# Kernel tuning notes

Measured on AMD Instinct MI355X. Metric: run time of the kernel, lower is better.

Reference implementation:

```python
import jax, jax.numpy as jnp
import numpy as np

N_CLUSTERS = 256  # must match fill_max of `clusters`
ALPHA = 7.18
MIN_MEMBERS = 4.0  # clusters with fewer members are dropped (as in original)


def setup_inputs() -> dict:
    key = jax.random.key(0)
    k1, k2 = jax.random.split(key)
    outputs = jax.random.normal(k1, (8192, 2048), dtype=jnp.float32)
    clusters = jax.random.randint(k2, (8192,), 0, N_CLUSTERS, dtype=jnp.int32)
    return {"outputs": outputs, "clusters": clusters}


def _magnet_loss(outputs, clusters):
    # outputs: [N, D] float32, clusters: [N] int32 in [0, N_CLUSTERS)
    n = outputs.shape[0]
    ones = jnp.ones((n,), jnp.float32)
    counts = jax.ops.segment_sum(ones, clusters, num_segments=N_CLUSTERS)          # [C]
    sums = jax.ops.segment_sum(outputs, clusters, num_segments=N_CLUSTERS)         # [C, D]
    means = sums / jnp.maximum(counts, 1.0)[:, None]                               # [C, D]
    valid = counts >= MIN_MEMBERS                                                   # [C] clusters kept
    inst_valid = valid[clusters]                                                    # [N]

    # residual norms to own-cluster mean (UNSQUARED L2, as in original)
    resid = outputs - means[clusters]                                               # [N, D]
    resid_norm = jnp.sqrt(jnp.sum(resid * resid, axis=1))                           # [N]

    num_instances = jnp.sum(jnp.where(valid, counts, 0.0))
    # original quirk: stdev = (sum of norms)^2 / num_instances
    stdev = jnp.square(jnp.sum(jnp.where(inst_valid, resid_norm, 0.0))) / num_instances

    # pairwise instance-to-mean L2 distances via GEMM: [N, C]
    sq = (jnp.sum(outputs * outputs, axis=1)[:, None]
          - 2.0 * (outputs @ means.T)
          + jnp.sum(means * means, axis=1)[None, :])
    dist = jnp.sqrt(jnp.maximum(sq, 0.0))                                           # [N, C]

    expd = jnp.exp(-0.5 * dist / stdev)                                             # [N, C]
    # denominator: sum over valid clusters other than own cluster
    other = jnp.arange(N_CLUSTERS, dtype=clusters.dtype)[None, :] != clusters[:, None]
    mask = valid[None, :] & other                                                   # [N, C]
    denom = jnp.sum(jnp.where(mask, expd, 0.0), axis=1)                             # [N]

    log_num = -0.5 * resid_norm / stdev - ALPHA                                     # [N]
    loss_i = jnp.log(denom) - log_num                                               # -log(exp(log_num)/denom)
    loss = jnp.sum(jnp.where(inst_valid, loss_i, 0.0)) / num_instances
    return loss.reshape(1)


def reference(outputs, clusters):
    return _magnet_loss(outputs.astype(jnp.float32), clusters)
```

## Files before the change

### kernel.cpp

```cpp
#include <hip/hip_runtime.h>
#include <hip/hip_bf16.h>
#include <math.h>

#define NROWS 8192
#define DIM   2048
#define NC    256
#define ALPHA_C 7.18f

typedef float  f32x4  __attribute__((ext_vector_type(4)));
typedef __bf16 bf16x8 __attribute__((ext_vector_type(8)));

#define OFF_A      (size_t)0
#define OFF_DOT    ((size_t)32 << 20)
#define OFF_B      ((size_t)40 << 20)
#define OFF_PERM   ((size_t)41 << 20)
#define OFF_MISC   (OFF_PERM + 32768)
#define OFF_GCTR   (OFF_MISC)
#define OFF_MN2    (OFF_MISC + 1024)
#define OFF_SCAL   (OFF_MISC + 2048)
#define OFF_HIST   (OFF_MISC + 3072)
#define OFF_CNT    (OFF_MISC + 4096)
#define OFF_BASE   (OFF_MISC + 5120)
#define OFF_ON2    (OFF_MISC + 6144)

__device__ __forceinline__ float wave_red_sum(float v) {
#pragma unroll
  for (int off = 32; off > 0; off >>= 1) v += __shfl_xor(v, off, 64);
  return v;
}

__global__ __launch_bounds__(256) void k_hist(const int* __restrict__ clu,
                                              int* __restrict__ hist) {
  __shared__ int h[NC];
  int tid = threadIdx.x;
  h[tid] = 0;
  __syncthreads();
  atomicAdd(&h[clu[blockIdx.x * 256 + tid]], 1);
  __syncthreads();
  if (h[tid]) atomicAdd(&hist[tid], h[tid]);
}

__global__ __launch_bounds__(256) void k_scan(const int* __restrict__ hist,
                                              float* __restrict__ counts,
                                              int* __restrict__ base,
                                              float* scal) {
  __shared__ int pre[NC];
  __shared__ float part[4];
  int tid = threadIdx.x;
  int c = hist[tid];
  counts[tid] = (float)c;
  pre[tid] = c;
  __syncthreads();
  for (int off = 1; off < NC; off <<= 1) {
    int v = (tid >= off) ? pre[tid - off] : 0;
    __syncthreads();
    pre[tid] += v;
    __syncthreads();
  }
  base[tid] = pre[tid] - c;
  float v = (c >= 4) ? (float)c : 0.0f;
  v = wave_red_sum(v);
  if ((tid & 63) == 0) part[tid >> 6] = v;
  __syncthreads();
  if (tid == 0) scal[1] = part[0] + part[1] + part[2] + part[3];
}

__global__ __launch_bounds__(256) void k_perm(const int* __restrict__ clu,
                                              const int* __restrict__ base,
                                              int* __restrict__ gctr,
                                              int* __restrict__ perm) {
  int i = blockIdx.x * 256 + threadIdx.x;
  int c = clu[i];
  int r = atomicAdd(&gctr[c], 1);
  perm[base[c] + r] = i;
}

__global__ __launch_bounds__(256) void k_msum(const float* __restrict__ out,
                                              const int* __restrict__ perm,
                                              const int* __restrict__ base,
                                              const float* __restrict__ counts,
                                              __bf16* __restrict__ B,
                                              float* __restrict__ mn2) {
  __shared__ int pr[64];
  __shared__ float part[4];
  int bid = blockIdx.x;
  int c = bid >> 3, sl = bid & 7;
  int tid = threadIdx.x;
  int col = sl * 256 + tid;
  int cnt = (int)counts[c];
  int b0 = base[c];
  float acc = 0.f;
  for (int r0 = 0; r0 < cnt; r0 += 64) {
    int lim = min(64, cnt - r0);
    if (tid < lim) pr[tid] = perm[b0 + r0 + tid];
    __syncthreads();
    for (int r = 0; r < lim; ++r) acc += out[(size_t)pr[r] * DIM + col];
    __syncthreads();
  }
  float mean = acc / fmaxf((float)cnt, 1.f);
  int nt = c >> 4, kk = col >> 5, lane = ((col >> 3) & 3) * 16 + (c & 15), j = col & 7;
  B[(((size_t)nt * 64 + kk) * 64 + lane) * 8 + j] = (__bf16)mean;
  float s = mean * mean;
  s = wave_red_sum(s);
  if ((tid & 63) == 0) part[tid >> 6] = s;
  __syncthreads();
  if (tid == 0) atomicAdd(&mn2[c], part[0] + part[1] + part[2] + part[3]);
}

__global__ __launch_bounds__(256) void k_conv(const float* __restrict__ out,
                                              bf16x8* __restrict__ A,
                                              float* __restrict__ onorm2) {
  __shared__ float lsum[256];
  int mt = blockIdx.x, tid = threadIdx.x;
  int r = tid & 15;
  const float* rowp = out + ((size_t)mt * 16 + r) * DIM;
  bf16x8* At = A + (size_t)mt * 4096;
  float acc = 0.f;
#pragma unroll 4
  for (int s = 0; s < 16; ++s) {
    int q = s * 256 + tid;
    int kk = q >> 6, lane = q & 63;
    int d = kk * 32 + (lane >> 4) * 8;
    const f32x4* src = (const f32x4*)(rowp + d);
    f32x4 v0 = src[0], v1 = src[1];
    bf16x8 b;
#pragma unroll
    for (int j = 0; j < 4; ++j) { float f = v0[j]; acc += f * f; b[j] = (__bf16)f; }
#pragma unroll
    for (int j = 0; j < 4; ++j) { float f = v1[j]; acc += f * f; b[4 + j] = (__bf16)f; }
    At[q] = b;
  }
  lsum[tid] = acc;
  __syncthreads();
  if (tid < 16) {
    float s = 0.f;
#pragma unroll
    for (int k = 0; k < 16; ++k) s += lsum[tid + 16 * k];
    onorm2[mt * 16 + tid] = s;
  }
}

__global__ __launch_bounds__(256) void k_gemm(const bf16x8* __restrict__ A,
                                              const bf16x8* __restrict__ B,
                                              float* __restrict__ dot) {
  int bid = blockIdx.x;
  int wg = (bid & 7) * 32 + (bid >> 3);
  int bm = wg >> 2, bn = wg & 3;
  int w = threadIdx.x >> 6, l = threadIdx.x & 63;
  int mt0 = bm * 8 + w * 2;
  int nt0 = bn * 4;
  const bf16x8* Ap = A + (size_t)mt0 * 64 * 64 + l;
  const bf16x8* Bp = B + (size_t)nt0 * 64 * 64 + l;
  f32x4 acc[2][4] = {};
  for (int kk = 0; kk < 64; ++kk) {
    bf16x8 a0 = Ap[kk * 64];
    bf16x8 a1 = Ap[4096 + kk * 64];
    bf16x8 b0 = Bp[kk * 64];
    bf16x8 b1 = Bp[4096 + kk * 64];
    bf16x8 b2 = Bp[8192 + kk * 64];
    bf16x8 b3 = Bp[12288 + kk * 64];
    acc[0][0] = __builtin_amdgcn_mfma_f32_16x16x32_bf16(a0, b0, acc[0][0], 0, 0, 0);
    acc[0][1] = __builtin_amdgcn_mfma_f32_16x16x32_bf16(a0, b1, acc[0][1], 0, 0, 0);
    acc[0][2] = __builtin_amdgcn_mfma_f32_16x16x32_bf16(a0, b2, acc[0][2], 0, 0, 0);
    acc[0][3] = __builtin_amdgcn_mfma_f32_16x16x32_bf16(a0, b3, acc[0][3], 0, 0, 0);
    acc[1][0] = __builtin_amdgcn_mfma_f32_16x16x32_bf16(a1, b0, acc[1][0], 0, 0, 0);
    acc[1][1] = __builtin_amdgcn_mfma_f32_16x16x32_bf16(a1, b1, acc[1][1], 0, 0, 0);
    acc[1][2] = __builtin_amdgcn_mfma_f32_16x16x32_bf16(a1, b2, acc[1][2], 0, 0, 0);
    acc[1][3] = __builtin_amdgcn_mfma_f32_16x16x32_bf16(a1, b3, acc[1][3], 0, 0, 0);
  }
  int r0 = bm * 128 + w * 32 + (l >> 4) * 4;
  int cb = bn * 64 + (l & 15);
#pragma unroll
  for (int m = 0; m < 2; ++m)
#pragma unroll
    for (int reg = 0; reg < 4; ++reg) {
      float* dst = dot + (size_t)(r0 + m * 16 + reg) * NC + cb;
#pragma unroll
      for (int n = 0; n < 4; ++n) dst[n * 16] = acc[m][n][reg];
    }
}

__global__ __launch_bounds__(256) void k_resid2(const float* __restrict__ dot,
                                                const int* __restrict__ clu,
                                                const float* __restrict__ onorm2,
                                                const float* __restrict__ mnorm2,
                                                const float* __restrict__ counts,
                                                float* scal) {
  __shared__ float part[4];
  int tid = threadIdx.x;
  int i = blockIdx.x * 256 + tid;
  int ci = clu[i];
  float dv = dot[(size_t)i * NC + ci];
  float rn = sqrtf(fmaxf(onorm2[i] - 2.f * dv + mnorm2[ci], 0.f));
  float v = (counts[ci] >= 4.0f) ? rn : 0.f;
  v = wave_red_sum(v);
  if ((tid & 63) == 0) part[tid >> 6] = v;
  __syncthreads();
  if (tid == 0) atomicAdd(&scal[0], part[0] + part[1] + part[2] + part[3]);
}

__global__ void k_stdev(float* scal) {
  scal[2] = scal[0] * scal[0] / scal[1];
}

__global__ __launch_bounds__(256) void k_denom(const float* __restrict__ dot,
                                               const int* __restrict__ clu,
                                               const float* __restrict__ on2v,
                                               const float* __restrict__ mn2,
                                               const float* __restrict__ counts,
                                               float* scal) {
  __shared__ float part[4];
  int w = threadIdx.x >> 6, l = threadIdx.x & 63;
  float cfac = -0.5f / scal[2];
  f32x4 mn = ((const f32x4*)mn2)[l];
  f32x4 cn = ((const f32x4*)counts)[l];
  float lsum = 0.f;
  int i0 = blockIdx.x * 32 + w * 8;
  for (int t = 0; t < 8; ++t) {
    int i = i0 + t;
    int ci = clu[i];
    float on2 = on2v[i];
    f32x4 dv = ((const f32x4*)(dot + (size_t)i * NC))[l];
    float dsum = 0.f;
#pragma unroll
    for (int j = 0; j < 4; ++j) {
      int cc = l * 4 + j;
      float dist = sqrtf(fmaxf(on2 - 2.f * dv[j] + mn[j], 0.f));
      float e = __expf(cfac * dist);
      dsum += ((cn[j] >= 4.0f) && (cc != ci)) ? e : 0.f;
    }
    dsum = wave_red_sum(dsum);
    if (l == 0 && counts[ci] >= 4.0f) {
      float dvi = dot[(size_t)i * NC + ci];
      float rn = sqrtf(fmaxf(on2 - 2.f * dvi + mn2[ci], 0.f));
      lsum += __logf(dsum) - (cfac * rn - ALPHA_C);
    }
  }
  lsum = wave_red_sum(lsum);
  if (l == 0) part[w] = lsum;
  __syncthreads();
  if (threadIdx.x == 0) atomicAdd(&scal[3], part[0] + part[1] + part[2] + part[3]);
}

__global__ void k_final(const float* scal, float* out) {
  out[0] = scal[3] / scal[1];
}

extern "C" void kernel_launch(void* const* d_in, const int* in_sizes, int n_in,
                              void* d_out, int out_size, void* d_ws, size_t ws_size,
                              hipStream_t stream) {
  const float* outputs = (const float*)d_in[0];
  const int* clusters = (const int*)d_in[1];
  float* out = (float*)d_out;
  char* ws = (char*)d_ws;

  bf16x8* A      = (bf16x8*)(ws + OFF_A);
  float*  dotb   = (float*)(ws + OFF_DOT);
  __bf16* B      = (__bf16*)(ws + OFF_B);
  int*    perm   = (int*)(ws + OFF_PERM);
  int*    gctr   = (int*)(ws + OFF_GCTR);
  float*  mn2    = (float*)(ws + OFF_MN2);
  float*  scal   = (float*)(ws + OFF_SCAL);
  int*    hist   = (int*)(ws + OFF_HIST);
  float*  counts = (float*)(ws + OFF_CNT);
  int*    base   = (int*)(ws + OFF_BASE);
  float*  on2    = (float*)(ws + OFF_ON2);

  hipMemsetAsync(ws + OFF_GCTR, 0, 4096, stream);
  k_hist<<<NROWS / 256, 256, 0, stream>>>(clusters, hist);
  k_scan<<<1, 256, 0, stream>>>(hist, counts, base, scal);
  k_perm<<<NROWS / 256, 256, 0, stream>>>(clusters, base, gctr, perm);
  k_conv<<<NROWS / 16, 256, 0, stream>>>(outputs, A, on2);
  k_msum<<<NC * 8, 256, 0, stream>>>(outputs, perm, base, counts, B, mn2);
  k_gemm<<<256, 256, 0, stream>>>(A, (const bf16x8*)B, dotb);
  k_resid2<<<NROWS / 256, 256, 0, stream>>>(dotb, clusters, on2, mn2, counts, scal);
  k_stdev<<<1, 1, 0, stream>>>(scal);
  k_denom<<<NROWS / 32, 256, 0, stream>>>(dotb, clusters, on2, mn2, counts, scal);
  k_final<<<1, 1, 0, stream>>>(scal, out);
}
```

Before: 179.4 us.

## Fuse GEMM, residual, denominator and final loss into one cooperative kernel

Replaces the GEMM, residual-norm, stdev, denominator and final kernels with a single cooperative kernel. It keeps the dot products in MFMA accumulator registers and uses grid syncs between the stdev reduction, the per-row denominator atomics and the final sum. This removes the 8192x256 float dot buffer write and reread, along with several launches. The histogram and scan are also merged into one single-block kernel. In exchange it adds three grid-wide barriers, per-row float atomics on dsum (which makes the sum order nondeterministic), and relies on all 256 blocks being co-resident.

New measurement: 262.3 us. +46.2%, slower.

```diff
diff --git a/kernel.cpp b/kernel.cpp
--- a/kernel.cpp
+++ b/kernel.cpp
@@ -1,6 +1,9 @@
 #include <hip/hip_runtime.h>
 #include <hip/hip_bf16.h>
+#include <hip/hip_cooperative_groups.h>
 #include <math.h>
+
+namespace cg = cooperative_groups;
 
 #define NROWS 8192
 #define DIM   2048
@@ -11,17 +14,18 @@
 typedef __bf16 bf16x8 __attribute__((ext_vector_type(8)));
 
 #define OFF_A      (size_t)0
-#define OFF_DOT    ((size_t)32 << 20)
-#define OFF_B      ((size_t)40 << 20)
-#define OFF_PERM   ((size_t)41 << 20)
-#define OFF_MISC   (OFF_PERM + 32768)
-#define OFF_GCTR   (OFF_MISC)
-#define OFF_MN2    (OFF_MISC + 1024)
-#define OFF_SCAL   (OFF_MISC + 2048)
-#define OFF_HIST   (OFF_MISC + 3072)
-#define OFF_CNT    (OFF_MISC + 4096)
-#define OFF_BASE   (OFF_MISC + 5120)
-#define OFF_ON2    (OFF_MISC + 6144)
+#define OFF_B      ((size_t)32 << 20)
+#define OFF_PERM   ((size_t)33 << 20)
+#define OFF_Z      (OFF_PERM + 32768)
+#define OFF_GCTR   (OFF_Z)
+#define OFF_MN2    (OFF_Z + 1024)
+#define OFF_SCAL   (OFF_Z + 2048)
+#define OFF_DSUM   (OFF_Z + 3072)
+#define ZSIZE      (3072 + 32768)
+#define OFF_CNT    (OFF_Z + ZSIZE)
+#define OFF_BASE   (OFF_CNT + 1024)
+#define OFF_ON2    (OFF_BASE + 1024)
+#define OFF_RN     (OFF_ON2 + 32768)
 
 __device__ __forceinline__ float wave_red_sum(float v) {
 #pragma unroll
@@ -29,25 +33,25 @@
   return v;
 }
 
-__global__ __launch_bounds__(256) void k_hist(const int* __restrict__ clu,
-                                              int* __restrict__ hist) {
-  __shared__ int h[NC];
-  int tid = threadIdx.x;
-  h[tid] = 0;
-  __syncthreads();
-  atomicAdd(&h[clu[blockIdx.x * 256 + tid]], 1);
-  __syncthreads();
-  if (h[tid]) atomicAdd(&hist[tid], h[tid]);
-}
-
-__global__ __launch_bounds__(256) void k_scan(const int* __restrict__ hist,
+__global__ __launch_bounds__(256) void k_prep(const int* __restrict__ clu,
                                               float* __restrict__ counts,
                                               int* __restrict__ base,
                                               float* scal) {
+  __shared__ int h[NC];
   __shared__ int pre[NC];
   __shared__ float part[4];
   int tid = threadIdx.x;
-  int c = hist[tid];
+  h[tid] = 0;
+  __syncthreads();
+  const int4* cl4 = (const int4*)clu;
+#pragma unroll
+  for (int s = 0; s < 8; ++s) {
+    int4 v = cl4[s * 256 + tid];
+    atomicAdd(&h[v.x], 1); atomicAdd(&h[v.y], 1);
+    atomicAdd(&h[v.z], 1); atomicAdd(&h[v.w], 1);
+  }
+  __syncthreads();
+  int c = h[tid];
   counts[tid] = (float)c;
   pre[tid] = c;
   __syncthreads();
@@ -73,6 +77,39 @@
   int c = clu[i];
   int r = atomicAdd(&gctr[c], 1);
   perm[base[c] + r] = i;
+}
+
+__global__ __launch_bounds__(256) void k_conv(const float* __restrict__ out,
+                                              bf16x8* __restrict__ A,
+                                              float* __restrict__ onorm2) {
+  __shared__ float lsum[256];
+  int mt = blockIdx.x, tid = threadIdx.x;
+  int r = tid & 15;
+  const float* rowp = out + ((size_t)mt * 16 + r) * DIM;
+  bf16x8* At = A + (size_t)mt * 4096;
+  float acc = 0.f;
+#pragma unroll 4
+  for (int s = 0; s < 16; ++s) {
+    int q = s * 256 + tid;
+    int kk = q >> 6, lane = q & 63;
+    int d = kk * 32 + (lane >> 4) * 8;
+    const f32x4* src = (const f32x4*)(rowp + d);
+    f32x4 v0 = src[0], v1 = src[1];
+    bf16x8 b;
+#pragma unroll
+    for (int j = 0; j < 4; ++j) { float f = v0[j]; acc += f * f; b[j] = (__bf16)f; }
+#pragma unroll
+    for (int j = 0; j < 4; ++j) { float f = v1[j]; acc += f * f; b[4 + j] = (__bf16)f; }
+    At[q] = b;
+  }
+  lsum[tid] = acc;
+  __syncthreads();
+  if (tid < 16) {
+    float s = 0.f;
+#pragma unroll
+    for (int k = 0; k < 16; ++k) s += lsum[tid + 16 * k];
+    onorm2[mt * 16 + tid] = s;
+  }
 }
 
 __global__ __launch_bounds__(256) void k_msum(const float* __restrict__ out,
@@ -107,42 +144,18 @@
   if (tid == 0) atomicAdd(&mn2[c], part[0] + part[1] + part[2] + part[3]);
 }
 
-__global__ __launch_bounds__(256) void k_conv(const float* __restrict__ out,
-                                              bf16x8* __restrict__ A,
-                                              float* __restrict__ onorm2) {
-  __shared__ float lsum[256];
-  int mt = blockIdx.x, tid = threadIdx.x;
-  int r = tid & 15;
-  const float* rowp = out + ((size_t)mt * 16 + r) * DIM;
-  bf16x8* At = A + (size_t)mt * 4096;
-  float acc = 0.f;
-#pragma unroll 4
-  for (int s = 0; s < 16; ++s) {
-    int q = s * 256 + tid;
-    int kk = q >> 6, lane = q & 63;
-    int d = kk * 32 + (lane >> 4) * 8;
-    const f32x4* src = (const f32x4*)(rowp + d);
-    f32x4 v0 = src[0], v1 = src[1];
-    bf16x8 b;
-#pragma unroll
-    for (int j = 0; j < 4; ++j) { float f = v0[j]; acc += f * f; b[j] = (__bf16)f; }
-#pragma unroll
-    for (int j = 0; j < 4; ++j) { float f = v1[j]; acc += f * f; b[4 + j] = (__bf16)f; }
-    At[q] = b;
-  }
-  lsum[tid] = acc;
-  __syncthreads();
-  if (tid < 16) {
-    float s = 0.f;
-#pragma unroll
-    for (int k = 0; k < 16; ++k) s += lsum[tid + 16 * k];
-    onorm2[mt * 16 + tid] = s;
-  }
-}
-
-__global__ __launch_bounds__(256) void k_gemm(const bf16x8* __restrict__ A,
-                                              const bf16x8* __restrict__ B,
-                                              float* __restrict__ dot) {
+__global__ __launch_bounds__(256) void k_fused(const bf16x8* __restrict__ A,
+                                               const bf16x8* __restrict__ B,
+                                               const int* __restrict__ clu,
+                                               const float* __restrict__ counts,
+                                               const float* __restrict__ on2v,
+                                               const float* __restrict__ mn2,
+                                               float* __restrict__ rn,
+                                               float* __restrict__ dsum,
+                                               float* scal,
+                                               float* outp) {
+  __shared__ float part[4];
+  cg::grid_group grid = cg::this_grid();
   int bid = blockIdx.x;
   int wg = (bid & 7) * 32 + (bid >> 3);
   int bm = wg >> 2, bn = wg & 3;
@@ -170,80 +183,78 @@
   }
   int r0 = bm * 128 + w * 32 + (l >> 4) * 4;
   int cb = bn * 64 + (l & 15);
+
+  int ciArr[8]; float on2Arr[8];
+  float rsum = 0.f;
 #pragma unroll
   for (int m = 0; m < 2; ++m)
 #pragma unroll
     for (int reg = 0; reg < 4; ++reg) {
-      float* dst = dot + (size_t)(r0 + m * 16 + reg) * NC + cb;
-#pragma unroll
-      for (int n = 0; n < 4; ++n) dst[n * 16] = acc[m][n][reg];
+      int idx = m * 4 + reg;
+      int i = r0 + m * 16 + reg;
+      int ci = clu[i];
+      float o2 = on2v[i];
+      ciArr[idx] = ci; on2Arr[idx] = o2;
+#pragma unroll
+      for (int n = 0; n < 4; ++n) {
+        int c = cb + n * 16;
+        if (c == ci) {
+          float v = acc[m][n][reg];
+          float rnv = sqrtf(fmaxf(o2 - 2.f * v + mn2[ci], 0.f));
+          rn[i] = rnv;
+          if (counts[ci] >= 4.f) rsum += rnv;
+        }
+      }
     }
-}
-
-__global__ __launch_bounds__(256) void k_resid2(const float* __restrict__ dot,
-                                                const int* __restrict__ clu,
-                                                const float* __restrict__ onorm2,
-                                                const float* __restrict__ mnorm2,
-                                                const float* __restrict__ counts,
-                                                float* scal) {
-  __shared__ float part[4];
+  rsum = wave_red_sum(rsum);
+  if (l == 0) part[w] = rsum;
+  __syncthreads();
+  if (threadIdx.x == 0) atomicAdd(&scal[0], part[0] + part[1] + part[2] + part[3]);
+  grid.sync();
+
+  float s0 = scal[0], s1 = scal[1];
+  float cfac = -0.5f * s1 / (s0 * s0);
+  float mnc[4], cnc[4];
+#pragma unroll
+  for (int n = 0; n < 4; ++n) { int c = cb + n * 16; mnc[n] = mn2[c]; cnc[n] = counts[c]; }
+#pragma unroll
+  for (int m = 0; m < 2; ++m)
+#pragma unroll
+    for (int reg = 0; reg < 4; ++reg) {
+      int idx = m * 4 + reg;
+      int i = r0 + m * 16 + reg;
+      int ci = ciArr[idx];
+      float o2 = on2Arr[idx];
+      float p = 0.f;
+#pragma unroll
+      for (int n = 0; n < 4; ++n) {
+        int c = cb + n * 16;
+        float v = acc[m][n][reg];
+        float dist = sqrtf(fmaxf(o2 - 2.f * v + mnc[n], 0.f));
+        float e = __expf(cfac * dist);
+        p += ((cnc[n] >= 4.f) && (c != ci)) ? e : 0.f;
+      }
+#pragma unroll
+      for (int off = 1; off < 16; off <<= 1) p += __shfl_xor(p, off, 64);
+      if ((l & 15) == 0) atomicAdd(&dsum[i], p);
+    }
+  grid.sync();
+
+  float lv = 0.f;
   int tid = threadIdx.x;
-  int i = blockIdx.x * 256 + tid;
-  int ci = clu[i];
-  float dv = dot[(size_t)i * NC + ci];
-  float rn = sqrtf(fmaxf(onorm2[i] - 2.f * dv + mnorm2[ci], 0.f));
-  float v = (counts[ci] >= 4.0f) ? rn : 0.f;
-  v = wave_red_sum(v);
-  if ((tid & 63) == 0) part[tid >> 6] = v;
-  __syncthreads();
-  if (tid == 0) atomicAdd(&scal[0], part[0] + part[1] + part[2] + part[3]);
-}
-
-__global__ void k_stdev(float* scal) {
-  scal[2] = scal[0] * scal[0] / scal[1];
-}
-
-__global__ __launch_bounds__(256) void k_denom(const float* __restrict__ dot,
-                                               const int* __restrict__ clu,
-                                               const float* __restrict__ on2v,
-                                               const float* __restrict__ mn2,
-                                               const float* __restrict__ counts,
-                                               float* scal) {
-  __shared__ float part[4];
-  int w = threadIdx.x >> 6, l = threadIdx.x & 63;
-  float cfac = -0.5f / scal[2];
-  f32x4 mn = ((const f32x4*)mn2)[l];
-  f32x4 cn = ((const f32x4*)counts)[l];
-  float lsum = 0.f;
-  int i0 = blockIdx.x * 32 + w * 8;
-  for (int t = 0; t < 8; ++t) {
-    int i = i0 + t;
+  if (tid < 32) {
+    int i = blockIdx.x * 32 + tid;
     int ci = clu[i];
-    float on2 = on2v[i];
-    f32x4 dv = ((const f32x4*)(dot + (size_t)i * NC))[l];
-    float dsum = 0.f;
-#pragma unroll
-    for (int j = 0; j < 4; ++j) {
-      int cc = l * 4 + j;
-      float dist = sqrtf(fmaxf(on2 - 2.f * dv[j] + mn[j], 0.f));
-      float e = __expf(cfac * dist);
-      dsum += ((cn[j] >= 4.0f) && (cc != ci)) ? e : 0.f;
-    }
-    dsum = wave_red_sum(dsum);
-    if (l == 0 && counts[ci] >= 4.0f) {
-      float dvi = dot[(size_t)i * NC + ci];
-      float rn = sqrtf(fmaxf(on2 - 2.f * dvi + mn2[ci], 0.f));
-      lsum += __logf(dsum) - (cfac * rn - ALPHA_C);
-    }
-  }
-  lsum = wave_red_sum(lsum);
-  if (l == 0) part[w] = lsum;
-  __syncthreads();
-  if (threadIdx.x == 0) atomicAdd(&scal[3], part[0] + part[1] + part[2] + part[3]);
-}
-
-__global__ void k_final(const float* scal, float* out) {
-  out[0] = scal[3] / scal[1];
+    if (counts[ci] >= 4.f)
+      lv = __logf(dsum[i]) - (cfac * rn[i] - ALPHA_C);
+  }
+  lv = wave_red_sum(lv);
+  if (l == 0) part[w] = lv;
+  __syncthreads();
+  if (tid == 0) atomicAdd(&scal[3], part[0] + part[1] + part[2] + part[3]);
+  grid.sync();
+
+  if (blockIdx.x == 0 && tid == 0) outp[0] = scal[3] / scal[1];
 }
 
 extern "C" void kernel_launch(void* const* d_in, const int* in_sizes, int n_in,
@@ -251,30 +262,29 @@
                               hipStream_t stream) {
   const float* outputs = (const float*)d_in[0];
   const int* clusters = (const int*)d_in[1];
-  float* out = (float*)d_out;
+  float* outp = (float*)d_out;
   char* ws = (char*)d_ws;
 
   bf16x8* A      = (bf16x8*)(ws + OFF_A);
-  float*  dotb   = (float*)(ws + OFF_DOT);
-  __bf16* B      = (__bf16*)(ws + OFF_B);
+  bf16x8* B      = (bf16x8*)(ws + OFF_B);
   int*    perm   = (int*)(ws + OFF_PERM);
   int*    gctr   = (int*)(ws + OFF_GCTR);
   float*  mn2    = (float*)(ws + OFF_MN2);
   float*  scal   = (float*)(ws + OFF_SCAL);
-  int*    hist   = (int*)(ws + OFF_HIST);
+  float*  dsum   = (float*)(ws + OFF_DSUM);
   float*  counts = (float*)(ws + OFF_CNT);
   int*    base   = (int*)(ws + OFF_BASE);
   float*  on2    = (float*)(ws + OFF_ON2);
-
-  hipMemsetAsync(ws + OFF_GCTR, 0, 4096, stream);
-  k_hist<<<NROWS / 256, 256, 0, stream>>>(clusters, hist);
-  k_scan<<<1, 256, 0, stream>>>(hist, counts, base, scal);
+  float*  rn     = (float*)(ws + OFF_RN);
+
+  hipMemsetAsync(ws + OFF_Z, 0, ZSIZE, stream);
+  k_prep<<<1, 256, 0, stream>>>(clusters, counts, base, scal);
   k_perm<<<NROWS / 256, 256, 0, stream>>>(clusters, base, gctr, perm);
   k_conv<<<NROWS / 16, 256, 0, stream>>>(outputs, A, on2);
-  k_msum<<<NC * 8, 256, 0, stream>>>(outputs, perm, base, counts, B, mn2);
-  k_gemm<<<256, 256, 0, stream>>>(A, (const bf16x8*)B, dotb);
-  k_resid2<<<NROWS / 256, 256, 0, stream>>>(dotb, clusters, on2, mn2, counts, scal);
-  k_stdev<<<1, 1, 0, stream>>>(scal);
-  k_denom<<<NROWS / 32, 256, 0, stream>>>(dotb, clusters, on2, mn2, counts, scal);
-  k_final<<<1, 1, 0, stream>>>(scal, out);
-}
+  k_msum<<<NC * 8, 256, 0, stream>>>(outputs, perm, base, counts, (__bf16*)B, mn2);
+
+  void* kargs[] = {(void*)&A, (void*)&B, (void*)&clusters, (void*)&counts,
+                   (void*)&on2, (void*)&mn2, (void*)&rn, (void*)&dsum,
+                   (void*)&scal, (void*)&outp};
+  hipLaunchCooperativeKernel((const void*)k_fused, dim3(256), dim3(256), kargs, 0, stream);
+}
```

## Fuse residual-norm reduction into GEMM epilogue and halve GEMM tile height

Applied to the files above, without the earlier changes.

The own-cluster residual-norm sum moves into the GEMM epilogue, using the accumulators still in registers, so the separate k_resid2 and k_stdev launches go away. k_denom now computes the stdev factor itself from scal[0] and scal[1]. The GEMM tile shrinks from 128 to 64 rows per block, which doubles the grid to 512 blocks to fill more CUs, at the cost of more B reloads. The epilogue adds per-lane branches and one atomic per block to the GEMM.

After: 172.2 us. 4.0% less time.

```diff
diff --git a/kernel.cpp b/kernel.cpp
--- a/kernel.cpp
+++ b/kernel.cpp
@@ -73,38 +73,6 @@
   int c = clu[i];
   int r = atomicAdd(&gctr[c], 1);
   perm[base[c] + r] = i;
-}
-
-__global__ __launch_bounds__(256) void k_msum(const float* __restrict__ out,
-                                              const int* __restrict__ perm,
-                                              const int* __restrict__ base,
-                                              const float* __restrict__ counts,
-                                              __bf16* __restrict__ B,
-                                              float* __restrict__ mn2) {
-  __shared__ int pr[64];
-  __shared__ float part[4];
-  int bid = blockIdx.x;
-  int c = bid >> 3, sl = bid & 7;
-  int tid = threadIdx.x;
-  int col = sl * 256 + tid;
-  int cnt = (int)counts[c];
-  int b0 = base[c];
-  float acc = 0.f;
-  for (int r0 = 0; r0 < cnt; r0 += 64) {
-    int lim = min(64, cnt - r0);
-    if (tid < lim) pr[tid] = perm[b0 + r0 + tid];
-    __syncthreads();
-    for (int r = 0; r < lim; ++r) acc += out[(size_t)pr[r] * DIM + col];
-    __syncthreads();
-  }
-  float mean = acc / fmaxf((float)cnt, 1.f);
-  int nt = c >> 4, kk = col >> 5, lane = ((col >> 3) & 3) * 16 + (c & 15), j = col & 7;
-  B[(((size_t)nt * 64 + kk) * 64 + lane) * 8 + j] = (__bf16)mean;
-  float s = mean * mean;
-  s = wave_red_sum(s);
-  if ((tid & 63) == 0) part[tid >> 6] = s;
-  __syncthreads();
-  if (tid == 0) atomicAdd(&mn2[c], part[0] + part[1] + part[2] + part[3]);
 }
 
 __global__ __launch_bounds__(256) void k_conv(const float* __restrict__ out,
@@ -140,67 +108,98 @@
   }
 }
 
+__global__ __launch_bounds__(256) void k_msum(const float* __restrict__ out,
+                                              const int* __restrict__ perm,
+                                              const int* __restrict__ base,
+                                              const float* __restrict__ counts,
+                                              __bf16* __restrict__ B,
+                                              float* __restrict__ mn2) {
+  __shared__ int pr[64];
+  __shared__ float part[4];
+  int bid = blockIdx.x;
+  int c = bid >> 3, sl = bid & 7;
+  int tid = threadIdx.x;
+  int col = sl * 256 + tid;
+  int cnt = (int)counts[c];
+  int b0 = base[c];
+  float acc = 0.f;
+  for (int r0 = 0; r0 < cnt; r0 += 64) {
+    int lim = min(64, cnt - r0);
+    if (tid < lim) pr[tid] = perm[b0 + r0 + tid];
+    __syncthreads();
+    for (int r = 0; r < lim; ++r) acc += out[(size_t)pr[r] * DIM + col];
+    __syncthreads();
+  }
+  float mean = acc / fmaxf((float)cnt, 1.f);
+  int nt = c >> 4, kk = col >> 5, lane = ((col >> 3) & 3) * 16 + (c & 15), j = col & 7;
+  B[(((size_t)nt * 64 + kk) * 64 + lane) * 8 + j] = (__bf16)mean;
+  float s = mean * mean;
+  s = wave_red_sum(s);
+  if ((tid & 63) == 0) part[tid >> 6] = s;
+  __syncthreads();
+  if (tid == 0) atomicAdd(&mn2[c], part[0] + part[1] + part[2] + part[3]);
+}
+
 __global__ __launch_bounds__(256) void k_gemm(const bf16x8* __restrict__ A,
                                               const bf16x8* __restrict__ B,
-                                              float* __restrict__ dot) {
+                                              const int* __restrict__ clu,
+                                              const float* __restrict__ counts,
+                                              const float* __restrict__ on2v,
+                                              const float* __restrict__ mn2,
+                                              float* __restrict__ dot,
+                                              float* scal) {
+  __shared__ float part[4];
   int bid = blockIdx.x;
-  int wg = (bid & 7) * 32 + (bid >> 3);
+  int wg = (bid & 7) * 64 + (bid >> 3);
   int bm = wg >> 2, bn = wg & 3;
   int w = threadIdx.x >> 6, l = threadIdx.x & 63;
-  int mt0 = bm * 8 + w * 2;
+  int mt = bm * 4 + w;
   int nt0 = bn * 4;
-  const bf16x8* Ap = A + (size_t)mt0 * 64 * 64 + l;
-  const bf16x8* Bp = B + (size_t)nt0 * 64 * 64 + l;
-  f32x4 acc[2][4] = {};
+  const bf16x8* Ap = A + (size_t)mt * 4096 + l;
+  const bf16x8* Bp = B + (size_t)nt0 * 4096 + l;
+  f32x4 acc[4] = {};
+#pragma unroll 2
   for (int kk = 0; kk < 64; ++kk) {
     bf16x8 a0 = Ap[kk * 64];
-    bf16x8 a1 = Ap[4096 + kk * 64];
     bf16x8 b0 = Bp[kk * 64];
     bf16x8 b1 = Bp[4096 + kk * 64];
     bf16x8 b2 = Bp[8192 + kk * 64];
     bf16x8 b3 = Bp[12288 + kk * 64];
-    acc[0][0] = __builtin_amdgcn_mfma_f32_16x16x32_bf16(a0, b0, acc[0][0], 0, 0, 0);
-    acc[0][1] = __builtin_amdgcn_mfma_f32_16x16x32_bf16(a0, b1, acc[0][1], 0, 0, 0);
-    acc[0][2] = __builtin_amdgcn_mfma_f32_16x16x32_bf16(a0, b2, acc[0][2], 0, 0, 0);
-    acc[0][3] = __builtin_amdgcn_mfma_f32_16x16x32_bf16(a0, b3, acc[0][3], 0, 0, 0);
-    acc[1][0] = __builtin_amdgcn_mfma_f32_16x16x32_bf16(a1, b0, acc[1][0], 0, 0, 0);
-    acc[1][1] = __builtin_amdgcn_mfma_f32_16x16x32_bf16(a1, b1, acc[1][1], 0, 0, 0);
-    acc[1][2] = __builtin_amdgcn_mfma_f32_16x16x32_bf16(a1, b2, acc[1][2], 0, 0, 0);
-    acc[1][3] = __builtin_amdgcn_mfma_f32_16x16x32_bf16(a1, b3, acc[1][3], 0, 0, 0);
-  }
-  int r0 = bm * 128 + w * 32 + (l >> 4) * 4;
+    acc[0] = __builtin_amdgcn_mfma_f32_16x16x32_bf16(a0, b0, acc[0], 0, 0, 0);
+    acc[1] = __builtin_amdgcn_mfma_f32_16x16x32_bf16(a0, b1, acc[1], 0, 0, 0);
+    acc[2] = __builtin_amdgcn_mfma_f32_16x16x32_bf16(a0, b2, acc[2], 0, 0, 0);
+    acc[3] = __builtin_amdgcn_mfma_f32_16x16x32_bf16(a0, b3, acc[3], 0, 0, 0);
+  }
+  int r0 = bm * 64 + w * 16 + (l >> 4) * 4;
   int cb = bn * 64 + (l & 15);
 #pragma unroll
-  for (int m = 0; m < 2; ++m)
-#pragma unroll
-    for (int reg = 0; reg < 4; ++reg) {
-      float* dst = dot + (size_t)(r0 + m * 16 + reg) * NC + cb;
-#pragma unroll
-      for (int n = 0; n < 4; ++n) dst[n * 16] = acc[m][n][reg];
+  for (int reg = 0; reg < 4; ++reg) {
+    float* dst = dot + (size_t)(r0 + reg) * NC + cb;
+    dst[0]  = acc[0][reg];
+    dst[16] = acc[1][reg];
+    dst[32] = acc[2][reg];
+    dst[48] = acc[3][reg];
+  }
+  float rsum = 0.f;
+#pragma unroll
+  for (int reg = 0; reg < 4; ++reg) {
+    int i = r0 + reg;
+    int ci = clu[i];
+#pragma unroll
+    for (int n = 0; n < 4; ++n) {
+      int c = cb + n * 16;
+      if (c == ci && counts[ci] >= 4.0f) {
+        rsum += sqrtf(fmaxf(on2v[i] - 2.f * acc[n][reg] + mn2[ci], 0.f));
+      }
     }
-}
-
-__global__ __launch_bounds__(256) void k_resid2(const float* __restrict__ dot,
-                                                const int* __restrict__ clu,
-                                                const float* __restrict__ onorm2,
-                                                const float* __restrict__ mnorm2,
-                                                const float* __restrict__ counts,
-                                                float* scal) {
-  __shared__ float part[4];
-  int tid = threadIdx.x;
-  int i = blockIdx.x * 256 + tid;
-  int ci = clu[i];
-  float dv = dot[(size_t)i * NC + ci];
-  float rn = sqrtf(fmaxf(onorm2[i] - 2.f * dv + mnorm2[ci], 0.f));
-  float v = (counts[ci] >= 4.0f) ? rn : 0.f;
-  v = wave_red_sum(v);
-  if ((tid & 63) == 0) part[tid >> 6] = v;
-  __syncthreads();
-  if (tid == 0) atomicAdd(&scal[0], part[0] + part[1] + part[2] + part[3]);
-}
-
-__global__ void k_stdev(float* scal) {
-  scal[2] = scal[0] * scal[0] / scal[1];
+  }
+  rsum = wave_red_sum(rsum);
+  if (l == 0) part[w] = rsum;
+  __syncthreads();
+  if (threadIdx.x == 0) {
+    float t = part[0] + part[1] + part[2] + part[3];
+    if (t != 0.f) atomicAdd(&scal[0], t);
+  }
 }
 
 __global__ __launch_bounds__(256) void k_denom(const float* __restrict__ dot,
@@ -211,7 +210,8 @@
                                                float* scal) {
   __shared__ float part[4];
   int w = threadIdx.x >> 6, l = threadIdx.x & 63;
-  float cfac = -0.5f / scal[2];
+  float s0 = scal[0], s1 = scal[1];
+  float cfac = -0.5f * s1 / (s0 * s0);
   f32x4 mn = ((const f32x4*)mn2)[l];
   f32x4 cn = ((const f32x4*)counts)[l];
   float lsum = 0.f;
@@ -272,9 +272,7 @@
   k_perm<<<NROWS / 256, 256, 0, stream>>>(clusters, base, gctr, perm);
   k_conv<<<NROWS / 16, 256, 0, stream>>>(outputs, A, on2);
   k_msum<<<NC * 8, 256, 0, stream>>>(outputs, perm, base, counts, B, mn2);
-  k_gemm<<<256, 256, 0, stream>>>(A, (const bf16x8*)B, dotb);
-  k_resid2<<<NROWS / 256, 256, 0, stream>>>(dotb, clusters, on2, mn2, counts, scal);
-  k_stdev<<<1, 1, 0, stream>>>(scal);
+  k_gemm<<<512, 256, 0, stream>>>(A, (const bf16x8*)B, clusters, counts, on2, mn2, dotb, scal);
   k_denom<<<NROWS / 32, 256, 0, stream>>>(dotb, clusters, on2, mn2, counts, scal);
   k_final<<<1, 1, 0, stream>>>(scal, out);
 }
```
